# Performance work log

Measured on AMD Instinct MI355X. Metric: run time of the kernel, lower is better.

Reference implementation:

```python
import jax, jax.numpy as jnp
import numpy as np

N = 1536       # n_nodes
D_IN = 256     # in_features
D_OUT = 64     # out_features (= n_hidden, n_heads=1, is_concat=True)
N_WAY = 16     # known_attacks_count
SLOPE = 0.2    # LeakyReLU negative slope


def setup_inputs() -> dict:
    key = jax.random.key(0)
    k1, k2, k3, k4, k5 = jax.random.split(key, 5)
    hidden_vectors = jax.random.normal(k1, (N, D_IN), dtype=jnp.float32)
    labels = jax.random.randint(k2, (N, 1), 0, N_WAY)
    zda_mask = jax.random.randint(k3, (N, 1), 0, 2).astype(bool)
    # deterministic support/query split: first half support, last half query
    query_mask = jnp.concatenate([jnp.zeros(N // 2, bool), jnp.ones(N // 2, bool)])
    W = jax.random.normal(k4, (D_OUT, D_IN), jnp.float32) * (1.0 / np.sqrt(D_IN))
    attn_w = jax.random.normal(k5, (D_OUT,), jnp.float32) * (1.0 / np.sqrt(D_OUT))
    return {"hidden_vectors": hidden_vectors, "W": W, "attn_w": attn_w,
            "labels": labels, "zda_mask": zda_mask, "query_mask": query_mask,
            "known_attacks_count": N_WAY}


def _forward(hidden_vectors, W, attn_w, labels, zda_mask, n_way):
    n = hidden_vectors.shape[0]
    dt = hidden_vectors.dtype
    # one-hot labels (scatter equivalent)
    oh = jax.nn.one_hot(labels[:, 0], n_way, dtype=dt)                 # [n, n_way]
    known = ~zda_mask[:, 0]                                            # unknown == zda
    ohm = jnp.where(known[:, None], oh, jnp.zeros((), dt))             # masked one-hot
    # collaborative kernel: semantic similarity between known pairs, else 1
    sem = ohm @ ohm.T                                                  # [n, n]
    cond = known[:, None] & known[None, :]
    kernel = jnp.where(cond, sem, jnp.ones((), dt))
    # GATv2 with shared weights, 1 head: e[i,j] = attn . lrelu(g[i] + g[j])
    g = hidden_vectors @ W.T                                           # [n, d_out]
    s = g[:, None, :] + g[None, :, :]                                  # [n, n, d_out]
    s = jnp.where(s >= 0, s, SLOPE * s)                                # LeakyReLU
    e = jnp.einsum('ijd,d->ij', s, attn_w)                             # [n, n]
    e = jnp.where(kernel == 0.0, -jnp.inf, e)                          # colaborative mask
    a = jax.nn.softmax(e, axis=1)                                      # [n, n]
    h_out = a @ g                                                      # [n, d_out] (concat, 1 head)
    # centroids over support nodes (first half)
    n_sup = n // 2
    h_sup, oh_sup = h_out[:n_sup], oh[:n_sup]
    agg = oh_sup.T @ h_sup                                             # [n_way, d_out]
    counts = oh_sup.sum(0)                                             # [n_way]
    centroids = jnp.where((counts > 0)[:, None],
                          agg / jnp.maximum(counts, 1.0)[:, None], 0.0)
    # inverse euclidean distance scores for query nodes (last half)
    hq = h_out[n_sup:]
    d2 = (jnp.sum(hq * hq, 1)[:, None] + jnp.sum(centroids * centroids, 1)[None, :]
          - 2.0 * hq @ centroids.T)
    dist = jnp.sqrt(jnp.maximum(d2, 0.0))
    scores = 1.0 / (dist + 1e-10)
    return scores, h_out, a


def reference(hidden_vectors, W, attn_w, labels, zda_mask, query_mask, known_attacks_count):
    return _forward(hidden_vectors, W, attn_w, labels, zda_mask, known_attacks_count)
```

## Files before the change

kernel.cpp:

```cpp
#include <hip/hip_runtime.h>
#include <math.h>

#define NN 1536
#define DIN 256
#define DOUT 64
#define NWAY 16
#define NSUP 768
#define IB 8
#define JBLK 256
#define SROWS 6

#define OFF_SCORES 0
#define OFF_H 12288
#define OFF_A 110592

#define WG 0
#define WQ 98304
#define WCODE 99840
#define WCENT 101376

__global__ __launch_bounds__(256) void k_g(const float* __restrict__ hid,
                                           const float* __restrict__ W,
                                           const float* __restrict__ attw,
                                           const int* __restrict__ labels,
                                           const int* __restrict__ zda,
                                           float* __restrict__ g,
                                           float* __restrict__ q,
                                           int* __restrict__ code) {
  int t = threadIdx.x;
  int r = t >> 6, d = t & 63;
  int i = blockIdx.x * 4 + r;
  const float4* hp = (const float4*)(hid + (size_t)i * DIN);
  const float4* wp = (const float4*)(W + (size_t)d * DIN);
  float4 acc = {0.f, 0.f, 0.f, 0.f};
#pragma unroll
  for (int k = 0; k < DIN / 4; k++) {
    float4 h4 = hp[k];
    float4 w4 = wp[k];
    acc.x = fmaf(h4.x, w4.x, acc.x);
    acc.y = fmaf(h4.y, w4.y, acc.y);
    acc.z = fmaf(h4.z, w4.z, acc.z);
    acc.w = fmaf(h4.w, w4.w, acc.w);
  }
  float gv = (acc.x + acc.y) + (acc.z + acc.w);
  g[(size_t)i * DOUT + d] = gv;
  float val = gv * attw[d];
#pragma unroll
  for (int off = 32; off >= 1; off >>= 1) val += __shfl_xor(val, off, 64);
  if (d == 0) q[i] = 0.6f * val;
  if (t < 4) {
    int ii = blockIdx.x * 4 + t;
    code[ii] = zda[ii] ? -1 : labels[ii];
  }
}

__global__ __launch_bounds__(256, 2) void k_e(const float* __restrict__ g,
                                              const float* __restrict__ q,
                                              const int* __restrict__ code,
                                              const float* __restrict__ attw,
                                              float* __restrict__ aout) {
  __shared__ float gis[IB * DOUT];
  __shared__ float lp[4][IB][JBLK];
  __shared__ float qi[IB];
  __shared__ int ci[IB];
  int t = threadIdx.x;
  int lane = t & 63;
  int w = t >> 6;
  int wq = __builtin_amdgcn_readfirstlane(w);
  int i0 = blockIdx.x * IB;
  int j0 = blockIdx.y * JBLK;

  if (t < IB * 16) {
    ((float4*)gis)[t] = ((const float4*)(g + (size_t)i0 * DOUT))[t];
  } else if (t < IB * 16 + IB) {
    int u = t - IB * 16;
    qi[u] = q[i0 + u];
    ci[u] = code[i0 + u];
  }
  float4 gj0[4], gj1[4], gj2[4], gj3[4];
  {
    const float4* p0 = (const float4*)(g + (size_t)(j0 + lane) * DOUT + wq * 16);
    const float4* p1 = (const float4*)(g + (size_t)(j0 + 64 + lane) * DOUT + wq * 16);
    const float4* p2 = (const float4*)(g + (size_t)(j0 + 128 + lane) * DOUT + wq * 16);
    const float4* p3 = (const float4*)(g + (size_t)(j0 + 192 + lane) * DOUT + wq * 16);
#pragma unroll
    for (int k = 0; k < 4; k++) gj0[k] = p0[k];
#pragma unroll
    for (int k = 0; k < 4; k++) gj1[k] = p1[k];
#pragma unroll
    for (int k = 0; k < 4; k++) gj2[k] = p2[k];
#pragma unroll
    for (int k = 0; k < 4; k++) gj3[k] = p3[k];
  }
  const float4* wv = (const float4*)(attw + wq * 16);
  __syncthreads();

#pragma unroll 1
  for (int u = 0; u < IB; u++) {
    const float4* gv = (const float4*)(gis + u * DOUT + wq * 16);
    float4 a0 = {0,0,0,0}, a1 = {0,0,0,0}, a2 = {0,0,0,0}, a3 = {0,0,0,0};
#pragma unroll
    for (int k = 0; k < 4; k++) {
      float4 a4 = gv[k];
      float4 w4 = wv[k];
      float4 b;
      b = gj0[k];
      a0.x = fmaf(w4.x, fabsf(a4.x + b.x), a0.x);
      a0.y = fmaf(w4.y, fabsf(a4.y + b.y), a0.y);
      a0.z = fmaf(w4.z, fabsf(a4.z + b.z), a0.z);
      a0.w = fmaf(w4.w, fabsf(a4.w + b.w), a0.w);
      b = gj1[k];
      a1.x = fmaf(w4.x, fabsf(a4.x + b.x), a1.x);
      a1.y = fmaf(w4.y, fabsf(a4.y + b.y), a1.y);
      a1.z = fmaf(w4.z, fabsf(a4.z + b.z), a1.z);
      a1.w = fmaf(w4.w, fabsf(a4.w + b.w), a1.w);
      b = gj2[k];
      a2.x = fmaf(w4.x, fabsf(a4.x + b.x), a2.x);
      a2.y = fmaf(w4.y, fabsf(a4.y + b.y), a2.y);
      a2.z = fmaf(w4.z, fabsf(a4.z + b.z), a2.z);
      a2.w = fmaf(w4.w, fabsf(a4.w + b.w), a2.w);
      b = gj3[k];
      a3.x = fmaf(w4.x, fabsf(a4.x + b.x), a3.x);
      a3.y = fmaf(w4.y, fabsf(a4.y + b.y), a3.y);
      a3.z = fmaf(w4.z, fabsf(a4.z + b.z), a3.z);
      a3.w = fmaf(w4.w, fabsf(a4.w + b.w), a3.w);
    }
    lp[w][u][lane] = (a0.x + a0.y) + (a0.z + a0.w);
    lp[w][u][lane + 64] = (a1.x + a1.y) + (a1.z + a1.w);
    lp[w][u][lane + 128] = (a2.x + a2.y) + (a2.z + a2.w);
    lp[w][u][lane + 192] = (a3.x + a3.y) + (a3.z + a3.w);
  }
  __syncthreads();

  int jg = j0 + t;
  float qj = q[jg];
  int cj = code[jg];
#pragma unroll
  for (int u = 0; u < IB; u++) {
    float s = (lp[0][u][t] + lp[1][u][t]) + (lp[2][u][t] + lp[3][u][t]);
    float e = (qi[u] + qj) + 0.4f * s;
    int cu = ci[u];
    if ((cu >= 0) && (cj >= 0) && (cu != cj)) e = -1e30f;
    aout[(size_t)(i0 + u) * NN + jg] = e;
  }
}

__global__ __launch_bounds__(1024) void k_smh(float* __restrict__ a,
                                              const float* __restrict__ g,
                                              float* __restrict__ h) {
  __shared__ float buf[64 * SROWS * 68];
  __shared__ float red[192];
  float* al = buf;
  int t = threadIdx.x;
  int lane = t & 63;
  int w = t >> 6;
  int r0 = blockIdx.x * SROWS;
  bool lo = (t < 512);

  float v0[SROWS], v1[SROWS], m[SROWS];
#pragma unroll
  for (int r = 0; r < SROWS; r++) {
    const float* row = a + (size_t)(r0 + r) * NN;
    v0[r] = row[t];
    v1[r] = lo ? row[1024 + t] : -3.0e38f;
  }
#pragma unroll
  for (int r = 0; r < SROWS; r++) {
    m[r] = fmaxf(v0[r], v1[r]);
#pragma unroll
    for (int off = 32; off >= 1; off >>= 1) m[r] = fmaxf(m[r], __shfl_xor(m[r], off, 64));
  }
  if (lane == 0) {
#pragma unroll
    for (int r = 0; r < SROWS; r++) red[w * SROWS + r] = m[r];
  }
  __syncthreads();
  float s[SROWS];
#pragma unroll
  for (int r = 0; r < SROWS; r++) {
    float mm = red[r];
#pragma unroll
    for (int k = 1; k < 16; k++) mm = fmaxf(mm, red[k * SROWS + r]);
    v0[r] = __expf(v0[r] - mm);
    v1[r] = lo ? __expf(v1[r] - mm) : 0.f;
    s[r] = v0[r] + v1[r];
#pragma unroll
    for (int off = 32; off >= 1; off >>= 1) s[r] += __shfl_xor(s[r], off, 64);
  }
  if (lane == 0) {
#pragma unroll
    for (int r = 0; r < SROWS; r++) red[96 + w * SROWS + r] = s[r];
  }
  __syncthreads();
#pragma unroll
  for (int r = 0; r < SROWS; r++) {
    float ss = red[96 + r];
#pragma unroll
    for (int k = 1; k < 16; k++) ss += red[96 + k * SROWS + r];
    float inv = 1.f / ss;
    float a0 = v0[r] * inv;
    al[r * NN + t] = a0;
    a[(size_t)(r0 + r) * NN + t] = a0;
    if (lo) {
      float a1 = v1[r] * inv;
      al[r * NN + 1024 + t] = a1;
      a[(size_t)(r0 + r) * NN + 1024 + t] = a1;
    }
  }
  __syncthreads();

  int jr = t >> 4;
  int dq = t & 15;
  float4 acc0 = {0,0,0,0}, acc1 = {0,0,0,0}, acc2 = {0,0,0,0};
  float4 acc3 = {0,0,0,0}, acc4 = {0,0,0,0}, acc5 = {0,0,0,0};
#pragma unroll 4
  for (int jj = 0; jj < NN / 64; jj++) {
    int j = jj * 64 + jr;
    float4 g4 = *(const float4*)(g + (size_t)j * DOUT + dq * 4);
    float a0 = al[j], a1 = al[NN + j], a2 = al[2 * NN + j];
    float a3 = al[3 * NN + j], a4 = al[4 * NN + j], a5 = al[5 * NN + j];
    acc0.x = fmaf(a0, g4.x, acc0.x); acc0.y = fmaf(a0, g4.y, acc0.y);
    acc0.z = fmaf(a0, g4.z, acc0.z); acc0.w = fmaf(a0, g4.w, acc0.w);
    acc1.x = fmaf(a1, g4.x, acc1.x); acc1.y = fmaf(a1, g4.y, acc1.y);
    acc1.z = fmaf(a1, g4.z, acc1.z); acc1.w = fmaf(a1, g4.w, acc1.w);
    acc2.x = fmaf(a2, g4.x, acc2.x); acc2.y = fmaf(a2, g4.y, acc2.y);
    acc2.z = fmaf(a2, g4.z, acc2.z); acc2.w = fmaf(a2, g4.w, acc2.w);
    acc3.x = fmaf(a3, g4.x, acc3.x); acc3.y = fmaf(a3, g4.y, acc3.y);
    acc3.z = fmaf(a3, g4.z, acc3.z); acc3.w = fmaf(a3, g4.w, acc3.w);
    acc4.x = fmaf(a4, g4.x, acc4.x); acc4.y = fmaf(a4, g4.y, acc4.y);
    acc4.z = fmaf(a4, g4.z, acc4.z); acc4.w = fmaf(a4, g4.w, acc4.w);
    acc5.x = fmaf(a5, g4.x, acc5.x); acc5.y = fmaf(a5, g4.y, acc5.y);
    acc5.z = fmaf(a5, g4.z, acc5.z); acc5.w = fmaf(a5, g4.w, acc5.w);
  }
  __syncthreads();
  *(float4*)(&buf[(jr * SROWS + 0) * 68 + dq * 4]) = acc0;
  *(float4*)(&buf[(jr * SROWS + 1) * 68 + dq * 4]) = acc1;
  *(float4*)(&buf[(jr * SROWS + 2) * 68 + dq * 4]) = acc2;
  *(float4*)(&buf[(jr * SROWS + 3) * 68 + dq * 4]) = acc3;
  *(float4*)(&buf[(jr * SROWS + 4) * 68 + dq * 4]) = acc4;
  *(float4*)(&buf[(jr * SROWS + 5) * 68 + dq * 4]) = acc5;
  __syncthreads();
  if (t < SROWS * DOUT) {
    int r = t >> 6, d = t & 63;
    float ssum = 0.f;
#pragma unroll
    for (int k = 0; k < 64; k++) ssum += buf[(k * SROWS + r) * 68 + d];
    h[(size_t)(r0 + r) * DOUT + d] = ssum;
  }
}

__global__ __launch_bounds__(1024) void k_cent(const float* __restrict__ h,
                                               const int* __restrict__ labels,
                                               float* __restrict__ cent) {
  __shared__ float part[16][64];
  __shared__ int pc[16];
  int c = blockIdx.x, t = threadIdx.x;
  int d = t & 63, rq = t >> 6;
  float acc = 0.f;
  int cnt = 0;
#pragma unroll 4
  for (int r = rq; r < NSUP; r += 16) {
    int lab = labels[r];
    if (lab == c) { acc += h[(size_t)r * DOUT + d]; cnt++; }
  }
  part[rq][d] = acc;
  if (d == 0) pc[rq] = cnt;
  __syncthreads();
  if (t < 64) {
    float num = 0.f;
    int count = 0;
#pragma unroll
    for (int k = 0; k < 16; k++) { num += part[k][t]; count += pc[k]; }
    cent[c * DOUT + t] = (count > 0) ? (num / (float)count) : 0.f;
  }
}

__global__ __launch_bounds__(256) void k_scores(const float* __restrict__ h,
                                                const float* __restrict__ cent,
                                                float* __restrict__ scores) {
  __shared__ float cl[NWAY * 65];
  __shared__ float hl[16 * 65];
  int t = threadIdx.x;
  int q0 = blockIdx.x * 16;
#pragma unroll
  for (int u = 0; u < 4; u++) {
    int f = t + u * 256;
    int row = f >> 6, k = f & 63;
    cl[row * 65 + k] = cent[f];
    hl[row * 65 + k] = h[(size_t)(NSUP + q0) * DOUT + f];
  }
  __syncthreads();
  int qr = t >> 4, c = t & 15;
  const float* hv = hl + qr * 65;
  const float* cv = cl + c * 65;
  float hh = 0.f, cc = 0.f, hc = 0.f;
#pragma unroll
  for (int k = 0; k < DOUT; k++) {
    float av = hv[k], bv = cv[k];
    hh = fmaf(av, av, hh);
    cc = fmaf(bv, bv, cc);
    hc = fmaf(av, bv, hc);
  }
  float d2 = fmaxf(hh + cc - 2.f * hc, 0.f);
  scores[q0 * NWAY + t] = 1.f / (sqrtf(d2) + 1e-10f);
}

extern "C" void kernel_launch(void* const* d_in, const int* in_sizes, int n_in,
                              void* d_out, int out_size, void* d_ws, size_t ws_size,
                              hipStream_t stream) {
  const float* hid = (const float*)d_in[0];
  const float* W = (const float*)d_in[1];
  const float* attw = (const float*)d_in[2];
  const int* labels = (const int*)d_in[3];
  const int* zda = (const int*)d_in[4];
  float* out = (float*)d_out;
  float* ws = (float*)d_ws;

  float* g = ws + WG;
  float* q = ws + WQ;
  int* code = (int*)(ws + WCODE);
  float* cent = ws + WCENT;
  float* scores = out + OFF_SCORES;
  float* h = out + OFF_H;
  float* a = out + OFF_A;

  hipLaunchKernelGGL(k_g, dim3(NN / 4), dim3(256), 0, stream, hid, W, attw, labels, zda, g, q, code);
  hipLaunchKernelGGL(k_e, dim3(NN / IB, NN / JBLK), dim3(256), 0, stream, g, q, code, attw, a);
  hipLaunchKernelGGL(k_smh, dim3(NN / SROWS), dim3(1024), 0, stream, a, g, h);
  hipLaunchKernelGGL(k_cent, dim3(NWAY), dim3(1024), 0, stream, h, labels, cent);
  hipLaunchKernelGGL(k_scores, dim3(NSUP / 16), dim3(256), 0, stream, h, cent, scores);
}
```

Baseline: 73.47 us.

## Fuse attention logits, softmax and aggregation into one kernel

Merges the logit kernel and the softmax+aggregation kernel into a single kernel. Each block computes six full rows of logits into LDS, applies the softmax there and runs the a@g reduction. This removes the global write and re-read of the unnormalized logit matrix and one kernel launch. In exchange it uses a large LDS footprint (about 140KB), one 1024-thread block per CU, and only 256 blocks with less parallelism in the logit phase.

```diff
diff --git a/kernel.cpp b/kernel.cpp
--- a/kernel.cpp
+++ b/kernel.cpp
@@ -6,9 +6,7 @@
 #define DOUT 64
 #define NWAY 16
 #define NSUP 768
-#define IB 8
-#define JBLK 256
-#define SROWS 6
+#define MR 6
 
 #define OFF_SCORES 0
 #define OFF_H 12288
@@ -54,157 +52,149 @@
   }
 }
 
-__global__ __launch_bounds__(256, 2) void k_e(const float* __restrict__ g,
-                                              const float* __restrict__ q,
-                                              const int* __restrict__ code,
-                                              const float* __restrict__ attw,
-                                              float* __restrict__ aout) {
-  __shared__ float gis[IB * DOUT];
-  __shared__ float lp[4][IB][JBLK];
-  __shared__ float qi[IB];
-  __shared__ int ci[IB];
+__global__ __launch_bounds__(1024) void k_mega(const float* __restrict__ g,
+                                               const float* __restrict__ q,
+                                               const int* __restrict__ code,
+                                               const float* __restrict__ attw,
+                                               float* __restrict__ aout,
+                                               float* __restrict__ hout) {
+  __shared__ float el[MR * NN];
+  __shared__ float buf2[26112];
+  __shared__ float gis[MR * DOUT];
+  __shared__ float qi[MR];
+  __shared__ int ci[MR];
+  __shared__ float red[192];
+
   int t = threadIdx.x;
   int lane = t & 63;
   int w = t >> 6;
-  int wq = __builtin_amdgcn_readfirstlane(w);
-  int i0 = blockIdx.x * IB;
-  int j0 = blockIdx.y * JBLK;
-
-  if (t < IB * 16) {
+  int wq = __builtin_amdgcn_readfirstlane(w & 3);
+  int jgrp = w >> 2;
+  int i0 = blockIdx.x * MR;
+  bool lo = (t < 512);
+
+  if (t < MR * 16) {
     ((float4*)gis)[t] = ((const float4*)(g + (size_t)i0 * DOUT))[t];
-  } else if (t < IB * 16 + IB) {
-    int u = t - IB * 16;
+  } else if (t < MR * 16 + MR) {
+    int u = t - MR * 16;
     qi[u] = q[i0 + u];
     ci[u] = code[i0 + u];
   }
-  float4 gj0[4], gj1[4], gj2[4], gj3[4];
+  const float4* wv = (const float4*)(attw + wq * 16);
+  __syncthreads();
+
+#pragma unroll 1
+  for (int p = 0; p < 2; p++) {
+    int jb = p * 768 + jgrp * 192;
+    float4 gj0[4], gj1[4], gj2[4];
+    {
+      const float4* p0 = (const float4*)(g + (size_t)(jb + lane) * DOUT + wq * 16);
+      const float4* p1 = (const float4*)(g + (size_t)(jb + 64 + lane) * DOUT + wq * 16);
+      const float4* p2 = (const float4*)(g + (size_t)(jb + 128 + lane) * DOUT + wq * 16);
+#pragma unroll
+      for (int k = 0; k < 4; k++) gj0[k] = p0[k];
+#pragma unroll
+      for (int k = 0; k < 4; k++) gj1[k] = p1[k];
+#pragma unroll
+      for (int k = 0; k < 4; k++) gj2[k] = p2[k];
+    }
+#pragma unroll 1
+    for (int u = 0; u < MR; u++) {
+      const float4* gv = (const float4*)(gis + u * DOUT + wq * 16);
+      float4 a0 = {0,0,0,0}, a1 = {0,0,0,0}, a2 = {0,0,0,0};
+#pragma unroll
+      for (int k = 0; k < 4; k++) {
+        float4 a4 = gv[k];
+        float4 w4 = wv[k];
+        float4 b;
+        b = gj0[k];
+        a0.x = fmaf(w4.x, fabsf(a4.x + b.x), a0.x);
+        a0.y = fmaf(w4.y, fabsf(a4.y + b.y), a0.y);
+        a0.z = fmaf(w4.z, fabsf(a4.z + b.z), a0.z);
+        a0.w = fmaf(w4.w, fabsf(a4.w + b.w), a0.w);
+        b = gj1[k];
+        a1.x = fmaf(w4.x, fabsf(a4.x + b.x), a1.x);
+        a1.y = fmaf(w4.y, fabsf(a4.y + b.y), a1.y);
+        a1.z = fmaf(w4.z, fabsf(a4.z + b.z), a1.z);
+        a1.w = fmaf(w4.w, fabsf(a4.w + b.w), a1.w);
+        b = gj2[k];
+        a2.x = fmaf(w4.x, fabsf(a4.x + b.x), a2.x);
+        a2.y = fmaf(w4.y, fabsf(a4.y + b.y), a2.y);
+        a2.z = fmaf(w4.z, fabsf(a4.z + b.z), a2.z);
+        a2.w = fmaf(w4.w, fabsf(a4.w + b.w), a2.w);
+      }
+      float* lpr = buf2 + (wq * MR + u) * 768 + jgrp * 192 + lane;
+      lpr[0]   = (a0.x + a0.y) + (a0.z + a0.w);
+      lpr[64]  = (a1.x + a1.y) + (a1.z + a1.w);
+      lpr[128] = (a2.x + a2.y) + (a2.z + a2.w);
+    }
+    __syncthreads();
+    if (t < 768) {
+      int jglob = p * 768 + t;
+      float qj = q[jglob];
+      int cj = code[jglob];
+#pragma unroll
+      for (int u = 0; u < MR; u++) {
+        float s = (buf2[(0 * MR + u) * 768 + t] + buf2[(1 * MR + u) * 768 + t]) +
+                  (buf2[(2 * MR + u) * 768 + t] + buf2[(3 * MR + u) * 768 + t]);
+        float e = (qi[u] + qj) + 0.4f * s;
+        int cu = ci[u];
+        if ((cu >= 0) && (cj >= 0) && (cu != cj)) e = -1e30f;
+        el[u * NN + jglob] = e;
+      }
+    }
+    __syncthreads();
+  }
+
   {
-    const float4* p0 = (const float4*)(g + (size_t)(j0 + lane) * DOUT + wq * 16);
-    const float4* p1 = (const float4*)(g + (size_t)(j0 + 64 + lane) * DOUT + wq * 16);
-    const float4* p2 = (const float4*)(g + (size_t)(j0 + 128 + lane) * DOUT + wq * 16);
-    const float4* p3 = (const float4*)(g + (size_t)(j0 + 192 + lane) * DOUT + wq * 16);
-#pragma unroll
-    for (int k = 0; k < 4; k++) gj0[k] = p0[k];
-#pragma unroll
-    for (int k = 0; k < 4; k++) gj1[k] = p1[k];
-#pragma unroll
-    for (int k = 0; k < 4; k++) gj2[k] = p2[k];
-#pragma unroll
-    for (int k = 0; k < 4; k++) gj3[k] = p3[k];
-  }
-  const float4* wv = (const float4*)(attw + wq * 16);
-  __syncthreads();
-
-#pragma unroll 1
-  for (int u = 0; u < IB; u++) {
-    const float4* gv = (const float4*)(gis + u * DOUT + wq * 16);
-    float4 a0 = {0,0,0,0}, a1 = {0,0,0,0}, a2 = {0,0,0,0}, a3 = {0,0,0,0};
-#pragma unroll
-    for (int k = 0; k < 4; k++) {
-      float4 a4 = gv[k];
-      float4 w4 = wv[k];
-      float4 b;
-      b = gj0[k];
-      a0.x = fmaf(w4.x, fabsf(a4.x + b.x), a0.x);
-      a0.y = fmaf(w4.y, fabsf(a4.y + b.y), a0.y);
-      a0.z = fmaf(w4.z, fabsf(a4.z + b.z), a0.z);
-      a0.w = fmaf(w4.w, fabsf(a4.w + b.w), a0.w);
-      b = gj1[k];
-      a1.x = fmaf(w4.x, fabsf(a4.x + b.x), a1.x);
-      a1.y = fmaf(w4.y, fabsf(a4.y + b.y), a1.y);
-      a1.z = fmaf(w4.z, fabsf(a4.z + b.z), a1.z);
-      a1.w = fmaf(w4.w, fabsf(a4.w + b.w), a1.w);
-      b = gj2[k];
-      a2.x = fmaf(w4.x, fabsf(a4.x + b.x), a2.x);
-      a2.y = fmaf(w4.y, fabsf(a4.y + b.y), a2.y);
-      a2.z = fmaf(w4.z, fabsf(a4.z + b.z), a2.z);
-      a2.w = fmaf(w4.w, fabsf(a4.w + b.w), a2.w);
-      b = gj3[k];
-      a3.x = fmaf(w4.x, fabsf(a4.x + b.x), a3.x);
-      a3.y = fmaf(w4.y, fabsf(a4.y + b.y), a3.y);
-      a3.z = fmaf(w4.z, fabsf(a4.z + b.z), a3.z);
-      a3.w = fmaf(w4.w, fabsf(a4.w + b.w), a3.w);
-    }
-    lp[w][u][lane] = (a0.x + a0.y) + (a0.z + a0.w);
-    lp[w][u][lane + 64] = (a1.x + a1.y) + (a1.z + a1.w);
-    lp[w][u][lane + 128] = (a2.x + a2.y) + (a2.z + a2.w);
-    lp[w][u][lane + 192] = (a3.x + a3.y) + (a3.z + a3.w);
-  }
-  __syncthreads();
-
-  int jg = j0 + t;
-  float qj = q[jg];
-  int cj = code[jg];
-#pragma unroll
-  for (int u = 0; u < IB; u++) {
-    float s = (lp[0][u][t] + lp[1][u][t]) + (lp[2][u][t] + lp[3][u][t]);
-    float e = (qi[u] + qj) + 0.4f * s;
-    int cu = ci[u];
-    if ((cu >= 0) && (cj >= 0) && (cu != cj)) e = -1e30f;
-    aout[(size_t)(i0 + u) * NN + jg] = e;
-  }
-}
-
-__global__ __launch_bounds__(1024) void k_smh(float* __restrict__ a,
-                                              const float* __restrict__ g,
-                                              float* __restrict__ h) {
-  __shared__ float buf[64 * SROWS * 68];
-  __shared__ float red[192];
-  float* al = buf;
-  int t = threadIdx.x;
-  int lane = t & 63;
-  int w = t >> 6;
-  int r0 = blockIdx.x * SROWS;
-  bool lo = (t < 512);
-
-  float v0[SROWS], v1[SROWS], m[SROWS];
-#pragma unroll
-  for (int r = 0; r < SROWS; r++) {
-    const float* row = a + (size_t)(r0 + r) * NN;
-    v0[r] = row[t];
-    v1[r] = lo ? row[1024 + t] : -3.0e38f;
-  }
-#pragma unroll
-  for (int r = 0; r < SROWS; r++) {
-    m[r] = fmaxf(v0[r], v1[r]);
-#pragma unroll
-    for (int off = 32; off >= 1; off >>= 1) m[r] = fmaxf(m[r], __shfl_xor(m[r], off, 64));
-  }
-  if (lane == 0) {
-#pragma unroll
-    for (int r = 0; r < SROWS; r++) red[w * SROWS + r] = m[r];
-  }
-  __syncthreads();
-  float s[SROWS];
-#pragma unroll
-  for (int r = 0; r < SROWS; r++) {
-    float mm = red[r];
-#pragma unroll
-    for (int k = 1; k < 16; k++) mm = fmaxf(mm, red[k * SROWS + r]);
-    v0[r] = __expf(v0[r] - mm);
-    v1[r] = lo ? __expf(v1[r] - mm) : 0.f;
-    s[r] = v0[r] + v1[r];
-#pragma unroll
-    for (int off = 32; off >= 1; off >>= 1) s[r] += __shfl_xor(s[r], off, 64);
-  }
-  if (lane == 0) {
-#pragma unroll
-    for (int r = 0; r < SROWS; r++) red[96 + w * SROWS + r] = s[r];
-  }
-  __syncthreads();
-#pragma unroll
-  for (int r = 0; r < SROWS; r++) {
-    float ss = red[96 + r];
-#pragma unroll
-    for (int k = 1; k < 16; k++) ss += red[96 + k * SROWS + r];
-    float inv = 1.f / ss;
-    float a0 = v0[r] * inv;
-    al[r * NN + t] = a0;
-    a[(size_t)(r0 + r) * NN + t] = a0;
-    if (lo) {
-      float a1 = v1[r] * inv;
-      al[r * NN + 1024 + t] = a1;
-      a[(size_t)(r0 + r) * NN + 1024 + t] = a1;
+    float v0[MR], v1[MR], m[MR];
+#pragma unroll
+    for (int r = 0; r < MR; r++) {
+      v0[r] = el[r * NN + t];
+      v1[r] = lo ? el[r * NN + 1024 + t] : -3.0e38f;
+    }
+#pragma unroll
+    for (int r = 0; r < MR; r++) {
+      m[r] = fmaxf(v0[r], v1[r]);
+#pragma unroll
+      for (int off = 32; off >= 1; off >>= 1) m[r] = fmaxf(m[r], __shfl_xor(m[r], off, 64));
+    }
+    if (lane == 0) {
+#pragma unroll
+      for (int r = 0; r < MR; r++) red[w * MR + r] = m[r];
+    }
+    __syncthreads();
+    float s[MR];
+#pragma unroll
+    for (int r = 0; r < MR; r++) {
+      float mm = red[r];
+#pragma unroll
+      for (int k = 1; k < 16; k++) mm = fmaxf(mm, red[k * MR + r]);
+      v0[r] = __expf(v0[r] - mm);
+      v1[r] = lo ? __expf(v1[r] - mm) : 0.f;
+      s[r] = v0[r] + v1[r];
+#pragma unroll
+      for (int off = 32; off >= 1; off >>= 1) s[r] += __shfl_xor(s[r], off, 64);
+    }
+    if (lane == 0) {
+#pragma unroll
+      for (int r = 0; r < MR; r++) red[96 + w * MR + r] = s[r];
+    }
+    __syncthreads();
+#pragma unroll
+    for (int r = 0; r < MR; r++) {
+      float ss = red[96 + r];
+#pragma unroll
+      for (int k = 1; k < 16; k++) ss += red[96 + k * MR + r];
+      float inv = 1.f / ss;
+      float a0 = v0[r] * inv;
+      el[r * NN + t] = a0;
+      aout[(size_t)(i0 + r) * NN + t] = a0;
+      if (lo) {
+        float a1 = v1[r] * inv;
+        el[r * NN + 1024 + t] = a1;
+        aout[(size_t)(i0 + r) * NN + 1024 + t] = a1;
+      }
     }
   }
   __syncthreads();
@@ -217,8 +207,8 @@
   for (int jj = 0; jj < NN / 64; jj++) {
     int j = jj * 64 + jr;
     float4 g4 = *(const float4*)(g + (size_t)j * DOUT + dq * 4);
-    float a0 = al[j], a1 = al[NN + j], a2 = al[2 * NN + j];
-    float a3 = al[3 * NN + j], a4 = al[4 * NN + j], a5 = al[5 * NN + j];
+    float a0 = el[j], a1 = el[NN + j], a2 = el[2 * NN + j];
+    float a3 = el[3 * NN + j], a4 = el[4 * NN + j], a5 = el[5 * NN + j];
     acc0.x = fmaf(a0, g4.x, acc0.x); acc0.y = fmaf(a0, g4.y, acc0.y);
     acc0.z = fmaf(a0, g4.z, acc0.z); acc0.w = fmaf(a0, g4.w, acc0.w);
     acc1.x = fmaf(a1, g4.x, acc1.x); acc1.y = fmaf(a1, g4.y, acc1.y);
@@ -232,20 +222,19 @@
     acc5.x = fmaf(a5, g4.x, acc5.x); acc5.y = fmaf(a5, g4.y, acc5.y);
     acc5.z = fmaf(a5, g4.z, acc5.z); acc5.w = fmaf(a5, g4.w, acc5.w);
   }
-  __syncthreads();
-  *(float4*)(&buf[(jr * SROWS + 0) * 68 + dq * 4]) = acc0;
-  *(float4*)(&buf[(jr * SROWS + 1) * 68 + dq * 4]) = acc1;
-  *(float4*)(&buf[(jr * SROWS + 2) * 68 + dq * 4]) = acc2;
-  *(float4*)(&buf[(jr * SROWS + 3) * 68 + dq * 4]) = acc3;
-  *(float4*)(&buf[(jr * SROWS + 4) * 68 + dq * 4]) = acc4;
-  *(float4*)(&buf[(jr * SROWS + 5) * 68 + dq * 4]) = acc5;
-  __syncthreads();
-  if (t < SROWS * DOUT) {
+  *(float4*)(&buf2[(jr * MR + 0) * 68 + dq * 4]) = acc0;
+  *(float4*)(&buf2[(jr * MR + 1) * 68 + dq * 4]) = acc1;
+  *(float4*)(&buf2[(jr * MR + 2) * 68 + dq * 4]) = acc2;
+  *(float4*)(&buf2[(jr * MR + 3) * 68 + dq * 4]) = acc3;
+  *(float4*)(&buf2[(jr * MR + 4) * 68 + dq * 4]) = acc4;
+  *(float4*)(&buf2[(jr * MR + 5) * 68 + dq * 4]) = acc5;
+  __syncthreads();
+  if (t < MR * DOUT) {
     int r = t >> 6, d = t & 63;
     float ssum = 0.f;
 #pragma unroll
-    for (int k = 0; k < 64; k++) ssum += buf[(k * SROWS + r) * 68 + d];
-    h[(size_t)(r0 + r) * DOUT + d] = ssum;
+    for (int k = 0; k < 64; k++) ssum += buf2[(k * MR + r) * 68 + d];
+    hout[(size_t)(i0 + r) * DOUT + d] = ssum;
   }
 }
 
@@ -325,8 +314,7 @@
   float* a = out + OFF_A;
 
   hipLaunchKernelGGL(k_g, dim3(NN / 4), dim3(256), 0, stream, hid, W, attw, labels, zda, g, q, code);
-  hipLaunchKernelGGL(k_e, dim3(NN / IB, NN / JBLK), dim3(256), 0, stream, g, q, code, attw, a);
-  hipLaunchKernelGGL(k_smh, dim3(NN / SROWS), dim3(1024), 0, stream, a, g, h);
+  hipLaunchKernelGGL(k_mega, dim3(NN / MR), dim3(1024), 0, stream, g, q, code, attw, a, h);
   hipLaunchKernelGGL(k_cent, dim3(NWAY), dim3(1024), 0, stream, h, labels, cent);
   hipLaunchKernelGGL(k_scores, dim3(NSUP / 16), dim3(256), 0, stream, h, cent, scores);
 }
```

Result: slower. 94.35 us (+28.4%).
